# Kernel optimization log

Measured on AMD Instinct MI355X. Metric: run time of the kernel, lower is better.

## Reference

```python
import jax, jax.numpy as jnp
import numpy as np

ALPHA = 0.2  # LeakyReLU negative slope
NEG_INF = -9e15


def setup_inputs() -> dict:
    key = jax.random.key(0)
    ks = jax.random.split(key, 6)
    B, N, F_in, F_out = 16, 1024, 1024, 512
    x = jax.random.normal(ks[0], (B, N, F_in), dtype=jnp.float32)
    adj = jax.random.randint(ks[1], (B, N, N), 0, 2, dtype=jnp.int32)
    W = jax.random.normal(ks[2], (F_in, F_out), dtype=jnp.float32) * 0.02
    a = jax.random.normal(ks[3], (2 * F_out, 1), dtype=jnp.float32) * 0.02
    fc_w = jax.random.normal(ks[4], (F_out, 2 * F_out), dtype=jnp.float32) * 0.02
    fc_b = jnp.zeros((F_out,), dtype=jnp.float32)
    return {"x": x, "adj": adj, "W": W, "a": a, "fc_w": fc_w, "fc_b": fc_b}


def reference(x, adj, W, a, fc_w, fc_b):
    # h: [B, N, F_out]
    h = jnp.matmul(x, W)
    F_out = W.shape[1]
    # The original builds a_input = concat(h_i, h_j) of shape [B,N,N,2F] and
    # contracts with a. Equivalently (same math, no O(N^2 F) intermediate):
    # e_ij = leakyrelu(h_i . a[:F] + h_j . a[F:])
    a1 = a[:F_out, 0]  # [F_out]
    a2 = a[F_out:, 0]  # [F_out]
    f1 = jnp.einsum('bnf,f->bn', h, a1)  # source term
    f2 = jnp.einsum('bnf,f->bn', h, a2)  # target term
    e = jax.nn.leaky_relu(f1[:, :, None] + f2[:, None, :], negative_slope=ALPHA)  # [B,N,N]
    attention = jnp.where(adj > 0, e, jnp.full_like(e, NEG_INF))
    attention = jax.nn.softmax(attention, axis=2)
    # dropout is identity in eval mode
    agg = jnp.matmul(attention, h)  # [B,N,F_out]
    h_prime = jnp.concatenate([agg, h], axis=2)  # [B,N,2F]
    h_prime = jnp.matmul(h_prime, fc_w.T) + fc_b
    return jax.nn.elu(h_prime)  # concat=True path
```

## Files before the change

### kernel.cpp

```cpp
#include <hip/hip_runtime.h>

#define ALPHA 0.2f

typedef __attribute__((ext_vector_type(8))) short short8;
typedef __attribute__((ext_vector_type(4))) float f32x4;

__device__ __forceinline__ unsigned short f2b(float f) {
  unsigned int u; __builtin_memcpy(&u, &f, 4);
  unsigned int r = (u + 0x7FFFu + ((u >> 16) & 1u)) >> 16;
  return (unsigned short)r;
}
__device__ __forceinline__ float b2f(unsigned short v) {
  unsigned int u = ((unsigned int)v) << 16; float f; __builtin_memcpy(&f, &u, 4); return f;
}
__device__ __forceinline__ void gl_lds16(const unsigned short* g, unsigned short* l) {
  __builtin_amdgcn_global_load_lds((__attribute__((address_space(1))) void*)g,
                                   (__attribute__((address_space(3))) void*)l, 16, 0, 0);
}

__device__ __forceinline__ void cvt_f4(const float* __restrict__ in,
                                       unsigned short* __restrict__ out,
                                       unsigned int f4idx) {
  float4 v = ((const float4*)in)[f4idx];
  alignas(8) unsigned short o[4];
  o[0] = f2b(v.x); o[1] = f2b(v.y); o[2] = f2b(v.z); o[3] = f2b(v.w);
  ((uint2*)out)[f4idx] = *(const uint2*)o;
}

__global__ __launch_bounds__(256) void prep1(const int* __restrict__ adj,
                                             unsigned short* __restrict__ bm16,
                                             const float* __restrict__ x,
                                             unsigned short* __restrict__ xb,
                                             const float* __restrict__ fcw,
                                             unsigned short* __restrict__ fcwb,
                                             const float* __restrict__ W,
                                             unsigned short* __restrict__ Wt) {
  __shared__ alignas(16) unsigned short tile[64][72];
  unsigned int bx = blockIdx.x;
  unsigned int tid = threadIdx.x;
  if (bx < 4096u) {
    unsigned int gw = bx * 4u + (tid >> 6);
    int lane = tid & 63;
    const int4* a4 = (const int4*)adj + (size_t)gw * 256;
    unsigned short* ob = bm16 + (size_t)gw * 64;
    #pragma unroll
    for (int t = 0; t < 4; t++) {
      int4 v = a4[t * 64 + lane];
      unsigned nib = (unsigned)(v.x > 0) | ((unsigned)(v.y > 0) << 1) |
                     ((unsigned)(v.z > 0) << 2) | ((unsigned)(v.w > 0) << 3);
      unsigned n1 = __shfl_down(nib, 1);
      unsigned n2 = __shfl_down(nib, 2);
      unsigned n3 = __shfl_down(nib, 3);
      if ((lane & 3) == 0)
        ob[t * 16 + (lane >> 2)] =
            (unsigned short)(nib | (n1 << 4) | (n2 << 8) | (n3 << 12));
    }
  } else if (bx < 12288u) {
    unsigned int base = (bx - 4096u) * 512u;
    cvt_f4(x, xb, base + tid);
    cvt_f4(x, xb, base + 256u + tid);
  } else if (bx < 12544u) {
    unsigned int base = (bx - 12288u) * 512u;
    cvt_f4(fcw, fcwb, base + tid);
    cvt_f4(fcw, fcwb, base + 256u + tid);
  } else {
    unsigned int idx = bx - 12544u;
    unsigned int k0 = (idx >> 3) * 64, n0 = (idx & 7) * 64;
    #pragma unroll
    for (int p = 0; p < 4; p++) {
      int r = p * 16 + (tid >> 4);
      int c = (tid & 15) * 4;
      float4 v = *(const float4*)(W + (size_t)(k0 + r) * 512 + n0 + c);
      tile[r][c] = f2b(v.x); tile[r][c + 1] = f2b(v.y);
      tile[r][c + 2] = f2b(v.z); tile[r][c + 3] = f2b(v.w);
    }
    __syncthreads();
    int f = tid >> 2;
    int ic = (tid & 3) * 16;
    alignas(16) unsigned short buf[16];
    #pragma unroll
    for (int k = 0; k < 16; k++) buf[k] = tile[ic + k][f];
    uint4* dst = (uint4*)(Wt + (size_t)(n0 + f) * 1024 + k0 + ic);
    dst[0] = ((const uint4*)buf)[0];
    dst[1] = ((const uint4*)buf)[1];
  }
}

__global__ __launch_bounds__(256) void prep2(const unsigned short* __restrict__ hp,
                                             const float* __restrict__ a,
                                             float* __restrict__ f1, float* __restrict__ f2,
                                             unsigned short* __restrict__ ht) {
  __shared__ alignas(16) unsigned short tile[64][72];
  int bx = blockIdx.x;
  int tid = threadIdx.x;
  if (bx < 4096) {
    int row = bx * 4 + (tid >> 6);
    int lane = tid & 63;
    const unsigned short* hrow = hp + (size_t)row * 1024 + 512;
    uint4 raw = *(const uint4*)(hrow + lane * 8);
    alignas(16) unsigned short hv[8]; __builtin_memcpy(hv, &raw, 16);
    float s1 = 0.f, s2 = 0.f;
    #pragma unroll
    for (int j = 0; j < 8; j++) {
      float hf = b2f(hv[j]);
      s1 += hf * a[lane * 8 + j];
      s2 += hf * a[512 + lane * 8 + j];
    }
    #pragma unroll
    for (int o = 32; o > 0; o >>= 1) { s1 += __shfl_down(s1, o); s2 += __shfl_down(s2, o); }
    if (lane == 0) { f1[row] = s1; f2[row] = s2; }
  } else {
    int idx = bx - 4096;
    int b = idx >> 7;
    int f0 = ((idx >> 4) & 7) * 64;
    int i0 = (idx & 15) * 64;
    #pragma unroll
    for (int p = 0; p < 2; p++) {
      int r = p * 32 + (tid >> 3);
      int c = (tid & 7) * 8;
      uint4 v = *(const uint4*)(hp + (size_t)(b * 1024 + i0 + r) * 1024 + 512 + f0 + c);
      *(uint4*)(&tile[r][c]) = v;
    }
    __syncthreads();
    int f = tid >> 2;
    int ic = (tid & 3) * 16;
    alignas(16) unsigned short buf[16];
    #pragma unroll
    for (int k = 0; k < 16; k++) buf[k] = tile[ic + k][f];
    uint4* dst = (uint4*)(ht + (size_t)(b * 512 + f0 + f) * 1024 + i0 + ic);
    dst[0] = ((const uint4*)buf)[0];
    dst[1] = ((const uint4*)buf)[1];
  }
}

__global__ __launch_bounds__(256) void rowsum_P(const unsigned short* __restrict__ bm16,
                                                const float* __restrict__ f1,
                                                const float* __restrict__ f2,
                                                float* __restrict__ invl,
                                                unsigned short* __restrict__ P) {
  int row = blockIdx.x * 4 + (threadIdx.x >> 6);
  int lane = threadIdx.x & 63;
  int b = row >> 10;
  float f1v = f1[row];
  unsigned int bits = bm16[(size_t)row * 64 + lane];
  const float* f2p = f2 + (b << 10) + lane * 16;
  float4 v0 = ((const float4*)f2p)[0];
  float4 v1 = ((const float4*)f2p)[1];
  float4 v2 = ((const float4*)f2p)[2];
  float4 v3 = ((const float4*)f2p)[3];
  float fv[16] = {v0.x, v0.y, v0.z, v0.w, v1.x, v1.y, v1.z, v1.w,
                  v2.x, v2.y, v2.z, v2.w, v3.x, v3.y, v3.z, v3.w};
  float s = 0.f;
  alignas(16) unsigned short o[16];
  #pragma unroll
  for (int j = 0; j < 16; j++) {
    float p = 0.f;
    if ((bits >> j) & 1u) {
      float z = f1v + fv[j];
      z = z > 0.f ? z : ALPHA * z;
      p = __expf(z);
      s += p;
    }
    o[j] = f2b(p);
  }
  uint4* dst = (uint4*)(P + (size_t)row * 1024 + lane * 16);
  dst[0] = ((const uint4*)o)[0];
  dst[1] = ((const uint4*)o)[1];
  #pragma unroll
  for (int off = 32; off > 0; off >>= 1) s += __shfl_down(s, off);
  if (lane == 0) invl[row] = 1.0f / s;
}

template <int EPI>
__global__ __launch_bounds__(256) void gemm_bt(
    const unsigned short* __restrict__ A, size_t aBS,
    const unsigned short* __restrict__ Bt, size_t bBS,
    int K,
    void* __restrict__ outp, size_t oBS, int ldo, int ocol,
    const float* __restrict__ scale,
    const float* __restrict__ bias) {
  __shared__ alignas(16) unsigned short As[2 * 128 * 64];
  __shared__ alignas(16) unsigned short Bs[2 * 128 * 64];
  const int tid = threadIdx.x;
  const int lane = tid & 63;
  const int w = tid >> 6;
  const int m0 = blockIdx.x * 128;
  const int n0 = blockIdx.y * 128;
  const int zb = blockIdx.z;
  const unsigned short* Ab = A + (size_t)zb * aBS;
  const unsigned short* Btb = Bt + (size_t)zb * bBS;

  f32x4 acc[4][4];
  #pragma unroll
  for (int i = 0; i < 4; i++)
    #pragma unroll
    for (int j = 0; j < 4; j++)
      #pragma unroll
      for (int r = 0; r < 4; r++) acc[i][j][r] = 0.f;

  const int lr = lane >> 3;
  const int lc = (lane & 7) ^ (lr & 7);
  const unsigned short* ag = Ab + (size_t)(m0 + w * 32 + lr) * K + lc * 8;
  const unsigned short* bg = Btb + (size_t)(n0 + w * 32 + lr) * K + lc * 8;
  const int sbase = w * 32 * 64;

  const int wm = (w & 1) * 64;
  const int wn = (w >> 1) * 64;
  const int row16 = lane & 15;
  const int quad = lane >> 4;
  const int sw = row16 & 7;

  #pragma unroll
  for (int t = 0; t < 4; t++) {
    gl_lds16(ag + (size_t)(t * 8) * K, As + sbase + t * 512);
    gl_lds16(bg + (size_t)(t * 8) * K, Bs + sbase + t * 512);
  }
  __syncthreads();

  int bufo = 0;
  for (int k0 = 0; k0 < K; k0 += 64) {
    const int nbufo = bufo ^ 8192;
    if (k0 + 64 < K) {
      #pragma unroll
      for (int t = 0; t < 4; t++) {
        gl_lds16(ag + (k0 + 64) + (size_t)(t * 8) * K, As + nbufo + sbase + t * 512);
        gl_lds16(bg + (k0 + 64) + (size_t)(t * 8) * K, Bs + nbufo + sbase + t * 512);
      }
    }
    short8 af[2][4], bf[2][4];
    #pragma unroll
    for (int s = 0; s < 2; s++) {
      #pragma unroll
      for (int i = 0; i < 4; i++) {
        af[s][i] = *(const short8*)(As + bufo + (wm + i * 16 + row16) * 64 + ((s * 4 + quad) ^ sw) * 8);
        bf[s][i] = *(const short8*)(Bs + bufo + (wn + i * 16 + row16) * 64 + ((s * 4 + quad) ^ sw) * 8);
      }
    }
    #pragma unroll
    for (int s = 0; s < 2; s++)
      #pragma unroll
      for (int am = 0; am < 4; am++)
        #pragma unroll
        for (int bn = 0; bn < 4; bn++)
          acc[am][bn] = __builtin_amdgcn_mfma_f32_16x16x32_bf16(af[s][am], bf[s][bn], acc[am][bn], 0, 0, 0);
    __syncthreads();
    bufo = nbufo;
  }

  const int col = lane & 15;
  const int r0 = quad * 4;
  #pragma unroll
  for (int am = 0; am < 4; am++) {
    #pragma unroll
    for (int bn = 0; bn < 4; bn++) {
      #pragma unroll
      for (int r = 0; r < 4; r++) {
        int m = m0 + wm + am * 16 + r0 + r;
        int n = n0 + wn + bn * 16 + col;
        float v = acc[am][bn][r];
        if (EPI == 3) v *= scale[zb * 1024 + m];
        if (EPI == 2) {
          v += bias[n];
          v = v > 0.f ? v : expm1f(v);
          ((float*)outp)[(size_t)m * ldo + n] = v;
        } else {
          ((unsigned short*)outp)[(size_t)zb * oBS + (size_t)m * ldo + ocol + n] = f2b(v);
        }
      }
    }
  }
}

extern "C" void kernel_launch(void* const* d_in, const int* in_sizes, int n_in,
                              void* d_out, int out_size, void* d_ws, size_t ws_size,
                              hipStream_t stream) {
  const float* x   = (const float*)d_in[0];
  const int*   adj = (const int*)d_in[1];
  const float* W   = (const float*)d_in[2];
  const float* a   = (const float*)d_in[3];
  const float* fcw = (const float*)d_in[4];
  const float* fcb = (const float*)d_in[5];
  float* out = (float*)d_out;
  char* ws = (char*)d_ws;

  unsigned short* xb   = (unsigned short*)(ws);
  unsigned short* hp   = (unsigned short*)(ws + 33554432);
  unsigned short* ht   = (unsigned short*)(ws + 67108864);
  unsigned short* Wt   = (unsigned short*)(ws + 83886080);
  unsigned short* fcwb = (unsigned short*)(ws + 84934656);
  float* f1            = (float*)(ws + 85983232);
  float* f2            = (float*)(ws + 86048768);
  float* invl          = (float*)(ws + 86114304);
  unsigned short* bm   = (unsigned short*)(ws + 86179840);
  unsigned short* P = xb;

  prep1<<<12672, 256, 0, stream>>>(adj, bm, x, xb, fcw, fcwb, W, Wt);

  gemm_bt<1><<<dim3(128, 4, 1), 256, 0, stream>>>(xb, 0, Wt, 0, 1024,
                                                  hp, 0, 1024, 512, nullptr, nullptr);
  prep2<<<6144, 256, 0, stream>>>(hp, a, f1, f2, ht);
  rowsum_P<<<4096, 256, 0, stream>>>(bm, f1, f2, invl, P);

  gemm_bt<3><<<dim3(8, 4, 16), 256, 0, stream>>>(P, 1024 * 1024, ht, 512 * 1024, 1024,
                                                 hp, 1024 * 1024, 1024, 0, invl, nullptr);
  gemm_bt<2><<<dim3(128, 4, 1), 256, 0, stream>>>(hp, 0, fcwb, 0, 1024,
                                                  out, 0, 512, 0, nullptr, fcb);
}
```

Measured before the change: 265.7 us.

## Drop adjacency bitmask pass and widen GEMM tiles with explicit-waitcnt pipelining

The separate adjacency-to-bitmask stage in prep1 is removed, and rowsum_P now reads the int32 adjacency directly, so one full pass over the adj array is no longer written and re-read. The GEMM kernel moves to 512 threads per block with 128x256 tiles and 8 waves. Its loop now issues the next stage of global-to-LDS loads right after the LDS reads, gated by raw s_waitcnt vmcnt/lgkmcnt plus s_barrier instead of __syncthreads, and raises wave priority around the MFMA block. This is meant to overlap memory traffic with MFMA work and halve the B-operand reloads per output, at the cost of larger LDS use and fragile manual wait counts.

New measurement: 259.0 us. -2.5%, faster.

```diff
diff --git a/kernel.cpp b/kernel.cpp
--- a/kernel.cpp
+++ b/kernel.cpp
@@ -17,6 +17,9 @@
   __builtin_amdgcn_global_load_lds((__attribute__((address_space(1))) void*)g,
                                    (__attribute__((address_space(3))) void*)l, 16, 0, 0);
 }
+__device__ __forceinline__ void vm6() { asm volatile("s_waitcnt vmcnt(6)" ::: "memory"); }
+__device__ __forceinline__ void vm0() { asm volatile("s_waitcnt vmcnt(0)" ::: "memory"); }
+__device__ __forceinline__ void lg0() { asm volatile("s_waitcnt lgkmcnt(0)" ::: "memory"); }
 
 __device__ __forceinline__ void cvt_f4(const float* __restrict__ in,
                                        unsigned short* __restrict__ out,
@@ -27,9 +30,7 @@
   ((uint2*)out)[f4idx] = *(const uint2*)o;
 }
 
-__global__ __launch_bounds__(256) void prep1(const int* __restrict__ adj,
-                                             unsigned short* __restrict__ bm16,
-                                             const float* __restrict__ x,
+__global__ __launch_bounds__(256) void prep1(const float* __restrict__ x,
                                              unsigned short* __restrict__ xb,
                                              const float* __restrict__ fcw,
                                              unsigned short* __restrict__ fcwb,
@@ -38,33 +39,16 @@
   __shared__ alignas(16) unsigned short tile[64][72];
   unsigned int bx = blockIdx.x;
   unsigned int tid = threadIdx.x;
-  if (bx < 4096u) {
-    unsigned int gw = bx * 4u + (tid >> 6);
-    int lane = tid & 63;
-    const int4* a4 = (const int4*)adj + (size_t)gw * 256;
-    unsigned short* ob = bm16 + (size_t)gw * 64;
-    #pragma unroll
-    for (int t = 0; t < 4; t++) {
-      int4 v = a4[t * 64 + lane];
-      unsigned nib = (unsigned)(v.x > 0) | ((unsigned)(v.y > 0) << 1) |
-                     ((unsigned)(v.z > 0) << 2) | ((unsigned)(v.w > 0) << 3);
-      unsigned n1 = __shfl_down(nib, 1);
-      unsigned n2 = __shfl_down(nib, 2);
-      unsigned n3 = __shfl_down(nib, 3);
-      if ((lane & 3) == 0)
-        ob[t * 16 + (lane >> 2)] =
-            (unsigned short)(nib | (n1 << 4) | (n2 << 8) | (n3 << 12));
-    }
-  } else if (bx < 12288u) {
-    unsigned int base = (bx - 4096u) * 512u;
+  if (bx < 8192u) {
+    unsigned int base = bx * 512u;
     cvt_f4(x, xb, base + tid);
     cvt_f4(x, xb, base + 256u + tid);
-  } else if (bx < 12544u) {
-    unsigned int base = (bx - 12288u) * 512u;
+  } else if (bx < 8448u) {
+    unsigned int base = (bx - 8192u) * 512u;
     cvt_f4(fcw, fcwb, base + tid);
     cvt_f4(fcw, fcwb, base + 256u + tid);
   } else {
-    unsigned int idx = bx - 12544u;
+    unsigned int idx = bx - 8448u;
     unsigned int k0 = (idx >> 3) * 64, n0 = (idx & 7) * 64;
     #pragma unroll
     for (int p = 0; p < 4; p++) {
@@ -133,7 +117,7 @@
   }
 }
 
-__global__ __launch_bounds__(256) void rowsum_P(const unsigned short* __restrict__ bm16,
+__global__ __launch_bounds__(256) void rowsum_P(const int* __restrict__ adj,
                                                 const float* __restrict__ f1,
                                                 const float* __restrict__ f2,
                                                 float* __restrict__ invl,
@@ -142,7 +126,13 @@
   int lane = threadIdx.x & 63;
   int b = row >> 10;
   float f1v = f1[row];
-  unsigned int bits = bm16[(size_t)row * 64 + lane];
+  const int4* ap = (const int4*)(adj + (size_t)row * 1024) + lane * 4;
+  int4 a0 = ap[0];
+  int4 a1 = ap[1];
+  int4 a2 = ap[2];
+  int4 a3 = ap[3];
+  int av[16] = {a0.x, a0.y, a0.z, a0.w, a1.x, a1.y, a1.z, a1.w,
+                a2.x, a2.y, a2.z, a2.w, a3.x, a3.y, a3.z, a3.w};
   const float* f2p = f2 + (b << 10) + lane * 16;
   float4 v0 = ((const float4*)f2p)[0];
   float4 v1 = ((const float4*)f2p)[1];
@@ -155,7 +145,7 @@
   #pragma unroll
   for (int j = 0; j < 16; j++) {
     float p = 0.f;
-    if ((bits >> j) & 1u) {
+    if (av[j] > 0) {
       float z = f1v + fv[j];
       z = z > 0.f ? z : ALPHA * z;
       p = __expf(z);
@@ -172,7 +162,7 @@
 }
 
 template <int EPI>
-__global__ __launch_bounds__(256) void gemm_bt(
+__global__ __launch_bounds__(512, 2) void gemm_bt(
     const unsigned short* __restrict__ A, size_t aBS,
     const unsigned short* __restrict__ Bt, size_t bBS,
     int K,
@@ -180,12 +170,12 @@
     const float* __restrict__ scale,
     const float* __restrict__ bias) {
   __shared__ alignas(16) unsigned short As[2 * 128 * 64];
-  __shared__ alignas(16) unsigned short Bs[2 * 128 * 64];
+  __shared__ alignas(16) unsigned short Bs[2 * 256 * 64];
   const int tid = threadIdx.x;
   const int lane = tid & 63;
   const int w = tid >> 6;
   const int m0 = blockIdx.x * 128;
-  const int n0 = blockIdx.y * 128;
+  const int n0 = blockIdx.y * 256;
   const int zb = blockIdx.z;
   const unsigned short* Ab = A + (size_t)zb * aBS;
   const unsigned short* Btb = Bt + (size_t)zb * bBS;
@@ -199,10 +189,11 @@
       for (int r = 0; r < 4; r++) acc[i][j][r] = 0.f;
 
   const int lr = lane >> 3;
-  const int lc = (lane & 7) ^ (lr & 7);
-  const unsigned short* ag = Ab + (size_t)(m0 + w * 32 + lr) * K + lc * 8;
-  const unsigned short* bg = Btb + (size_t)(n0 + w * 32 + lr) * K + lc * 8;
-  const int sbase = w * 32 * 64;
+  const int lc = (lane & 7) ^ lr;
+  const unsigned short* ag = Ab + (size_t)(m0 + w * 8 + lr) * K + lc * 8;
+  const unsigned short* bg = Btb + (size_t)(n0 + w * 8 + lr) * K + lc * 8;
+  const int asb = w * 8 * 64;
+  const int bsb = w * 8 * 64;
 
   const int wm = (w & 1) * 64;
   const int wn = (w >> 1) * 64;
@@ -210,32 +201,52 @@
   const int quad = lane >> 4;
   const int sw = row16 & 7;
 
-  #pragma unroll
-  for (int t = 0; t < 4; t++) {
-    gl_lds16(ag + (size_t)(t * 8) * K, As + sbase + t * 512);
-    gl_lds16(bg + (size_t)(t * 8) * K, Bs + sbase + t * 512);
-  }
-  __syncthreads();
-
-  int bufo = 0;
-  for (int k0 = 0; k0 < K; k0 += 64) {
-    const int nbufo = bufo ^ 8192;
-    if (k0 + 64 < K) {
-      #pragma unroll
-      for (int t = 0; t < 4; t++) {
-        gl_lds16(ag + (k0 + 64) + (size_t)(t * 8) * K, As + nbufo + sbase + t * 512);
-        gl_lds16(bg + (k0 + 64) + (size_t)(t * 8) * K, Bs + nbufo + sbase + t * 512);
+  const int nk = K >> 6;
+
+  #pragma unroll
+  for (int t = 0; t < 2; t++)
+    gl_lds16(ag + (size_t)(t * 64) * K, As + t * 4096 + asb);
+  #pragma unroll
+  for (int t = 0; t < 4; t++)
+    gl_lds16(bg + (size_t)(t * 64) * K, Bs + t * 4096 + bsb);
+  #pragma unroll
+  for (int t = 0; t < 2; t++)
+    gl_lds16(ag + 64 + (size_t)(t * 64) * K, As + 8192 + t * 4096 + asb);
+  #pragma unroll
+  for (int t = 0; t < 4; t++)
+    gl_lds16(bg + 64 + (size_t)(t * 64) * K, Bs + 16384 + t * 4096 + bsb);
+  vm6();
+  __builtin_amdgcn_s_barrier();
+
+  for (int k = 0; k < nk; k++) {
+    const int ab = (k & 1) * 8192;
+    const int bb = (k & 1) * 16384;
+    const bool st2 = (k + 2 < nk);
+    const bool pub = (k + 1 < nk);
+
+    short8 af[2][4], bf[2][4];
+    #pragma unroll
+    for (int s = 0; s < 2; s++) {
+      #pragma unroll
+      for (int i = 0; i < 4; i++) {
+        af[s][i] = *(const short8*)(As + ab + (wm + i * 16 + row16) * 64 + ((s * 4 + quad) ^ sw) * 8);
+        bf[s][i] = *(const short8*)(Bs + bb + (wn + i * 16 + row16) * 64 + ((s * 4 + quad) ^ sw) * 8);
       }
     }
-    short8 af[2][4], bf[2][4];
-    #pragma unroll
-    for (int s = 0; s < 2; s++) {
-      #pragma unroll
-      for (int i = 0; i < 4; i++) {
-        af[s][i] = *(const short8*)(As + bufo + (wm + i * 16 + row16) * 64 + ((s * 4 + quad) ^ sw) * 8);
-        bf[s][i] = *(const short8*)(Bs + bufo + (wn + i * 16 + row16) * 64 + ((s * 4 + quad) ^ sw) * 8);
-      }
-    }
+    lg0();
+    __builtin_amdgcn_s_barrier();
+
+    if (st2) {
+      const int ko = (k + 2) * 64;
+      #pragma unroll
+      for (int t = 0; t < 2; t++)
+        gl_lds16(ag + ko + (size_t)(t * 64) * K, As + ab + t * 4096 + asb);
+      #pragma unroll
+      for (int t = 0; t < 4; t++)
+        gl_lds16(bg + ko + (size_t)(t * 64) * K, Bs + bb + t * 4096 + bsb);
+    }
+
+    __builtin_amdgcn_s_setprio(1);
     #pragma unroll
     for (int s = 0; s < 2; s++)
       #pragma unroll
@@ -243,8 +254,12 @@
         #pragma unroll
         for (int bn = 0; bn < 4; bn++)
           acc[am][bn] = __builtin_amdgcn_mfma_f32_16x16x32_bf16(af[s][am], bf[s][bn], acc[am][bn], 0, 0, 0);
-    __syncthreads();
-    bufo = nbufo;
+    __builtin_amdgcn_s_setprio(0);
+
+    if (pub) {
+      if (st2) vm6(); else vm0();
+      __builtin_amdgcn_s_barrier();
+    }
   }
 
   const int col = lane & 15;
@@ -291,18 +306,17 @@
   float* f1            = (float*)(ws + 85983232);
   float* f2            = (float*)(ws + 86048768);
   float* invl          = (float*)(ws + 86114304);
-  unsigned short* bm   = (unsigned short*)(ws + 86179840);
   unsigned short* P = xb;
 
-  prep1<<<12672, 256, 0, stream>>>(adj, bm, x, xb, fcw, fcwb, W, Wt);
-
-  gemm_bt<1><<<dim3(128, 4, 1), 256, 0, stream>>>(xb, 0, Wt, 0, 1024,
+  prep1<<<8576, 256, 0, stream>>>(x, xb, fcw, fcwb, W, Wt);
+
+  gemm_bt<1><<<dim3(128, 2, 1), 512, 0, stream>>>(xb, 0, Wt, 0, 1024,
                                                   hp, 0, 1024, 512, nullptr, nullptr);
   prep2<<<6144, 256, 0, stream>>>(hp, a, f1, f2, ht);
-  rowsum_P<<<4096, 256, 0, stream>>>(bm, f1, f2, invl, P);
-
-  gemm_bt<3><<<dim3(8, 4, 16), 256, 0, stream>>>(P, 1024 * 1024, ht, 512 * 1024, 1024,
+  rowsum_P<<<4096, 256, 0, stream>>>(adj, f1, f2, invl, P);
+
+  gemm_bt<3><<<dim3(8, 2, 16), 512, 0, stream>>>(P, 1024 * 1024, ht, 512 * 1024, 1024,
                                                  hp, 1024 * 1024, 1024, 0, invl, nullptr);
-  gemm_bt<2><<<dim3(128, 4, 1), 256, 0, stream>>>(hp, 0, fcwb, 0, 1024,
+  gemm_bt<2><<<dim3(128, 2, 1), 512, 0, stream>>>(hp, 0, fcwb, 0, 1024,
                                                   out, 0, 512, 0, nullptr, fcb);
 }
```
